# Kernel tuning notes

Measured on AMD Instinct MI355X. Metric: run time of the kernel, lower is better.

## Reference

```python
import jax, jax.numpy as jnp
import numpy as np

EMB = 1024
HEADS = 16
HD = EMB // HEADS

def setup_inputs() -> dict:
    key = jax.random.key(0)
    ks = jax.random.split(key, 9)
    s = 1.0 / np.sqrt(EMB)
    x = jax.random.normal(ks[0], (4, 2048, EMB), dtype=jnp.float32)
    Wq = jax.random.uniform(ks[1], (EMB, EMB), jnp.float32, -s, s)
    bq = jax.random.uniform(ks[2], (EMB,), jnp.float32, -s, s)
    Wk = jax.random.uniform(ks[3], (EMB, EMB), jnp.float32, -s, s)
    bk = jax.random.uniform(ks[4], (EMB,), jnp.float32, -s, s)
    Wv = jax.random.uniform(ks[5], (EMB, EMB), jnp.float32, -s, s)
    bv = jax.random.uniform(ks[6], (EMB,), jnp.float32, -s, s)
    Wo = jax.random.uniform(ks[7], (EMB, EMB), jnp.float32, -s, s)
    bo = jax.random.uniform(ks[8], (EMB,), jnp.float32, -s, s)
    return {"x": x, "Wq": Wq, "bq": bq, "Wk": Wk, "bk": bk, "Wv": Wv, "bv": bv, "Wo": Wo, "bo": bo}

def reference(x, Wq, bq, Wk, bk, Wv, bv, Wo, bo):
    B, T, C = x.shape
    # projections (torch Linear: y = x @ W^T + b)
    q = (x @ Wq.T + bq).reshape(B, T, HEADS, HD).transpose(0, 2, 1, 3)  # [B,H,T,hd]
    k = (x @ Wk.T + bk).reshape(B, T, HEADS, HD).transpose(0, 2, 1, 3)
    v = (x @ Wv.T + bv).reshape(B, T, HEADS, HD).transpose(0, 2, 1, 3)
    scores = jnp.einsum('bhqd,bhkd->bhqk', q, k) / jnp.sqrt(jnp.float32(HD))
    weights = jax.nn.softmax(scores, axis=-1)
    attn = jnp.einsum('bhqk,bhkd->bhqd', weights, v)
    out = attn.transpose(0, 2, 1, 3).reshape(B, T, C)
    return out @ Wo.T + bo
```

## Files before the change

kernel.cpp:

```cpp
#include <hip/hip_runtime.h>

#define TSEQ  2048
#define BATCH 4
#define NHEAD 16
#define EMB   1024

typedef __attribute__((ext_vector_type(8))) __bf16 bf16x8;
typedef __attribute__((ext_vector_type(4))) __bf16 bf16x4;
typedef __attribute__((ext_vector_type(4))) float  floatx4;
typedef __attribute__((ext_vector_type(2))) unsigned int uint32x2;
typedef __attribute__((ext_vector_type(4))) unsigned int uint32x4;

__device__ __forceinline__ void gload_lds16(const __bf16* g, __bf16* lds_uniform_base) {
  __builtin_amdgcn_global_load_lds(
      (__attribute__((address_space(1))) void*)(g),
      (__attribute__((address_space(3))) void*)(lds_uniform_base),
      16, 0, 0);
}

__global__ __launch_bounds__(256) void cvt_f32_bf16(
    const float* __restrict__ src, __bf16* __restrict__ dst)
{
  const int gid = (blockIdx.x * 256 + threadIdx.x) * 4;
  const float4 v = *(const float4*)(src + gid);
  dst[gid + 0] = (__bf16)v.x;
  dst[gid + 1] = (__bf16)v.y;
  dst[gid + 2] = (__bf16)v.z;
  dst[gid + 3] = (__bf16)v.w;
}

__global__ __launch_bounds__(256) void cvt_w4(
    const float* __restrict__ s0, const float* __restrict__ s1,
    const float* __restrict__ s2, const float* __restrict__ s3,
    __bf16* __restrict__ d0, __bf16* __restrict__ d1,
    __bf16* __restrict__ d2, __bf16* __restrict__ d3)
{
  const int z = blockIdx.z;
  const float* src = (z == 0) ? s0 : (z == 1) ? s1 : (z == 2) ? s2 : s3;
  __bf16*      dst = (z == 0) ? d0 : (z == 1) ? d1 : (z == 2) ? d2 : d3;
  const int gid = (blockIdx.x * 256 + threadIdx.x) * 4;
  const float4 v = *(const float4*)(src + gid);
  dst[gid + 0] = (__bf16)v.x;
  dst[gid + 1] = (__bf16)v.y;
  dst[gid + 2] = (__bf16)v.z;
  dst[gid + 3] = (__bf16)v.w;
}

#define GQ_NT 16

#define G2_STAGE(BUF, T)                                                                  \
  {                                                                                       \
    _Pragma("unroll")                                                                     \
    for (int c = 0; c < 4; c++)                                                           \
      gload_lds16(aStage + (size_t)(c * 64) * 1024 + (T) * 64,                            \
                  &As[BUF][(c * 64 + wid * 8) * 64]);                                     \
    _Pragma("unroll")                                                                     \
    for (int c = 0; c < 2; c++)                                                           \
      gload_lds16(bStage + (size_t)(c * 64) * 1024 + (T) * 64,                            \
                  &Bs[BUF][(c * 64 + wid * 8) * 64]);                                     \
  }

#define G2_AF(I, H) (*(const bf16x8*)(&As[cur][(wm * 64 + (I) * 16 + l16) * 64 + (((H) * 4 + quad) ^ h7) * 8]))
#define G2_BF(J, H) (*(const bf16x8*)(&Bs[cur][(wn * 64 + (J) * 16 + l16) * 64 + (((H) * 4 + quad) ^ h7) * 8]))

#define G2_MFMA_PAIR(I, J)                                                                \
  acc[I][J] = __builtin_amdgcn_mfma_f32_16x16x32_bf16(af[I][0], bfr[J][0], acc[I][J], 0, 0, 0); \
  acc[I][J] = __builtin_amdgcn_mfma_f32_16x16x32_bf16(af[I][1], bfr[J][1], acc[I][J], 0, 0, 0);

#define GEMM2_BODY(C_STORE)                                                               \
  const int tid  = threadIdx.x;                                                           \
  const int lane = tid & 63;                                                              \
  const int wid  = tid >> 6;                                                    \
  const int l16  = lane & 15;                                                             \
  const int quad = lane >> 4;                                                             \
  const int wm   = wid >> 1;                                        \
  const int wn   = wid & 1;                                         \
  const int lin  = blockIdx.x + blockIdx.y * 8;                                           \
  const int swz  = (lin & 7) * 32 + (lin >> 3);                                           \
  const int m0   = (swz >> 3) * 256;                                                      \
  const int n0   = (swz & 7) * 128;                                                       \
  __shared__ alignas(16) __bf16 As[2][256 * 64];                                          \
  __shared__ alignas(16) __bf16 Bs[2][128 * 64];                                          \
  floatx4 acc[4][4];                                                                      \
  _Pragma("unroll")                                                                       \
  for (int i = 0; i < 4; i++)                                                             \
    _Pragma("unroll")                                                                     \
    for (int j = 0; j < 4; j++) acc[i][j] = (floatx4){0.f, 0.f, 0.f, 0.f};                \
  const int lrow = lane >> 3;                                                             \
  const int xsg  = (lane & 7) ^ lrow;                                                     \
  const __bf16* aStage = A + (size_t)(m0 + wid * 8 + lrow) * 1024 + xsg * 8;              \
  const __bf16* bStage = W + (size_t)(n0 + wid * 8 + lrow) * 1024 + xsg * 8;              \
  const int h7 = l16 & 7;                                                                 \
  G2_STAGE(0, 0)                                                                          \
  G2_STAGE(1, 1)                                                                          \
  __asm__ __volatile__("s_waitcnt vmcnt(6)\n\ts_barrier" ::: "memory");                   \
  int cur = 0;                                                                            \
  _Pragma("unroll 1")                                                                     \
  for (int t = 0; t < GQ_NT; ++t) {                                                       \
    bf16x8 af[4][2], bfr[4][2];                                                           \
                                    \
    af[0][0] = G2_AF(0, 0);  af[0][1] = G2_AF(0, 1);                                      \
    af[1][0] = G2_AF(1, 0);  af[1][1] = G2_AF(1, 1);                                      \
    bfr[0][0] = G2_BF(0, 0); bfr[0][1] = G2_BF(0, 1);                                     \
    bfr[1][0] = G2_BF(1, 0); bfr[1][1] = G2_BF(1, 1);                                     \
    __builtin_amdgcn_s_setprio(1);                                                        \
    G2_MFMA_PAIR(0, 0) G2_MFMA_PAIR(0, 1) G2_MFMA_PAIR(1, 0) G2_MFMA_PAIR(1, 1)          \
    __builtin_amdgcn_s_setprio(0);                                                        \
    __asm__ __volatile__("s_barrier" ::: "memory");                                       \
                           \
    bfr[2][0] = G2_BF(2, 0); bfr[2][1] = G2_BF(2, 1);                                     \
    bfr[3][0] = G2_BF(3, 0); bfr[3][1] = G2_BF(3, 1);                                     \
    __builtin_amdgcn_s_setprio(1);                                                        \
    G2_MFMA_PAIR(0, 2) G2_MFMA_PAIR(0, 3) G2_MFMA_PAIR(1, 2) G2_MFMA_PAIR(1, 3)          \
    __builtin_amdgcn_s_setprio(0);                                                        \
    __asm__ __volatile__("s_barrier" ::: "memory");                                       \
                           \
    af[2][0] = G2_AF(2, 0);  af[2][1] = G2_AF(2, 1);                                      \
    af[3][0] = G2_AF(3, 0);  af[3][1] = G2_AF(3, 1);                                      \
    __builtin_amdgcn_s_setprio(1);                                                        \
    G2_MFMA_PAIR(2, 0) G2_MFMA_PAIR(2, 1) G2_MFMA_PAIR(3, 0) G2_MFMA_PAIR(3, 1)          \
    __builtin_amdgcn_s_setprio(0);                                                        \
    __asm__ __volatile__("s_barrier" ::: "memory");                                       \
                 \
                 \
    if (t + 2 < GQ_NT) { G2_STAGE(cur, t + 2) }                                           \
    __builtin_amdgcn_s_setprio(1);                                                        \
    G2_MFMA_PAIR(2, 2) G2_MFMA_PAIR(2, 3) G2_MFMA_PAIR(3, 2) G2_MFMA_PAIR(3, 3)          \
    __builtin_amdgcn_s_setprio(0);                                                        \
    if (t + 2 < GQ_NT) {                                                                  \
      __asm__ __volatile__("s_waitcnt vmcnt(6)\n\ts_barrier" ::: "memory");               \
    } else if (t + 1 < GQ_NT) {                                                           \
      __asm__ __volatile__("s_waitcnt vmcnt(0)\n\ts_barrier" ::: "memory");               \
    }                                                                                     \
    cur ^= 1;                                                                             \
  }                                                                                       \
  float bv[4];                                                                            \
  _Pragma("unroll")                                                                       \
  for (int j = 0; j < 4; j++) bv[j] = Bb[n0 + wn * 64 + j * 16 + l16];                    \
  _Pragma("unroll")                                                                       \
  for (int i = 0; i < 4; i++) {                                                           \
    const size_t mrow = (size_t)m0 + wm * 64 + i * 16 + quad * 4;                         \
    _Pragma("unroll")                                                                     \
    for (int j = 0; j < 4; j++) {                                                         \
      const int col = n0 + wn * 64 + j * 16 + l16;                                        \
      _Pragma("unroll")                                                                   \
      for (int r = 0; r < 4; r++) C_STORE;                                                \
    }                                                                                     \
  }

__global__ __launch_bounds__(512, 2) void gemm_bt_bias(
    const __bf16* __restrict__ A,
    const __bf16* __restrict__ W0, const __bf16* __restrict__ W1, const __bf16* __restrict__ W2,
    const float* __restrict__ B0, const float* __restrict__ B1, const float* __restrict__ B2,
    __bf16* __restrict__ C0, __bf16* __restrict__ C1, __bf16* __restrict__ C2)
{
  const int z = blockIdx.z;
  const __bf16* W  = (z == 0) ? W0 : ((z == 1) ? W1 : W2);
  const float*  Bb = (z == 0) ? B0 : ((z == 1) ? B1 : B2);
  __bf16*       C  = (z == 0) ? C0 : ((z == 1) ? C1 : C2);
  const float  scl = (z == 0) ? 0.125f * 1.44269504088896340736f : 1.0f;
  GEMM2_BODY(C[(mrow + r) * 1024 + col] = (__bf16)((acc[i][j][r] + bv[j]) * scl))
}

__global__ __launch_bounds__(512, 2) void gemm_bt_bias_f32(
    const __bf16* __restrict__ A, const __bf16* __restrict__ W,
    const float* __restrict__ Bb, float* __restrict__ C)
{
  GEMM2_BODY(C[(mrow + r) * 1024 + col] = acc[i][j][r] + bv[j])
}

__global__ __launch_bounds__(256) void v_transpose(
    const __bf16* __restrict__ V, __bf16* __restrict__ VT)
{
  const int t0 = blockIdx.x * 64;
  const int bh = blockIdx.y;
  const int b  = bh >> 4;
  const int h  = bh & 15;
  const int tid = threadIdx.x;

  __shared__ alignas(16) __bf16 Ls[64 * 72];

  const int row = tid >> 2, seg = tid & 3;
  const __bf16* src = V + ((size_t)(b * TSEQ + t0 + row)) * EMB + h * 64;
  *(bf16x8*)(&Ls[row * 72 + seg * 8])       = *(const bf16x8*)(src + seg * 8);
  *(bf16x8*)(&Ls[row * 72 + (seg + 4) * 8]) = *(const bf16x8*)(src + (seg + 4) * 8);
  __syncthreads();

  const int od = tid >> 2, oseg = tid & 3;
  bf16x8 o0, o1;
#pragma unroll
  for (int j = 0; j < 8; j++) o0[j] = Ls[(oseg * 16 + j) * 72 + od];
#pragma unroll
  for (int j = 0; j < 8; j++) o1[j] = Ls[(oseg * 16 + 8 + j) * 72 + od];
  __bf16* dst = VT + ((size_t)bh * 64 + od) * TSEQ + t0 + oseg * 16;
  *(bf16x8*)(dst)     = o0;
  *(bf16x8*)(dst + 8) = o1;
}

#define KVB 64
#define NT  (TSEQ / KVB)

#define FA_ZERO (floatx4){0.f, 0.f, 0.f, 0.f}

#define FA_STAGE(BUF, TILE)                                                               \
  if ((TILE) < NT) {                                                                      \
    _Pragma("unroll")                                                                     \
    for (int c = 0; c < 2; c++) {                                                         \
      gload_lds16(kstage + (size_t)((TILE) * KVB + c * 8) * EMB,                          \
                  &Ks[BUF][(wid * 16 + c * 8) * 64]);                                     \
      gload_lds16(vstage + (size_t)(c * 8) * TSEQ + (TILE) * KVB,                         \
                  &VTs[BUF][(wid * 16 + c * 8) * 64]);                                    \
    }                                                                                     \
  }

#define SM_PACK(TA, TB, DST)                                                              \
  {                                                                                       \
    bf16x4 pa_, pb_;                                                                      \
    _Pragma("unroll")                                                                     \
    for (int r = 0; r < 4; r++) pa_[r] = (__bf16)__builtin_amdgcn_exp2f((TA)[r]);         \
    _Pragma("unroll")                                                                     \
    for (int r = 0; r < 4; r++) pb_[r] = (__bf16)__builtin_amdgcn_exp2f((TB)[r]);         \
    const uint32x2 A2_ = __builtin_bit_cast(uint32x2, pa_);                               \
    const uint32x2 B2_ = __builtin_bit_cast(uint32x2, pb_);                               \
    const uint32x2 r0_ = __builtin_amdgcn_permlane32_swap(A2_.x, B2_.x, false, false);    \
    const uint32x2 r1_ = __builtin_amdgcn_permlane32_swap(A2_.y, B2_.y, false, false);    \
    const uint32x2 s0_ = __builtin_amdgcn_permlane16_swap(r0_.x, r0_.y, false, false);    \
    const uint32x2 s1_ = __builtin_amdgcn_permlane16_swap(r1_.x, r1_.y, false, false);    \
    const uint32x4 fw_ = (uint32x4){s0_.x, s1_.x, s0_.y, s1_.y};                          \
    DST = __builtin_bit_cast(bf16x8, fw_);                                                \
  }

#define QK_BLOCK(BUF, KS, TA, TB)                                                         \
  {                                                                                       \
    const bf16x8 ka0 = *(const bf16x8*)(&Ks[BUF][(KS) * 2048 + aoff0]);                   \
    const bf16x8 ka1 = *(const bf16x8*)(&Ks[BUF][(KS) * 2048 + aoff1]);                   \
    const bf16x8 kb0 = *(const bf16x8*)(&Ks[BUF][(KS) * 2048 + 1024 + aoff0]);            \
    const bf16x8 kb1 = *(const bf16x8*)(&Ks[BUF][(KS) * 2048 + 1024 + aoff1]);            \
    _Pragma("unroll")                                                                     \
    for (int g = 0; g < 4; g++) {                                                         \
      TA[g] = FA_ZERO;                                                                    \
      TA[g] = __builtin_amdgcn_mfma_f32_16x16x32_bf16(ka0, qf[g][0], TA[g], 0, 0, 0);     \
      TA[g] = __builtin_amdgcn_mfma_f32_16x16x32_bf16(ka1, qf[g][1], TA[g], 0, 0, 0);     \
      TB[g] = FA_ZERO;                                                                    \
      TB[g] = __builtin_amdgcn_mfma_f32_16x16x32_bf16(kb0, qf[g][0], TB[g], 0, 0, 0);     \
      TB[g] = __builtin_amdgcn_mfma_f32_16x16x32_bf16(kb1, qf[g][1], TB[g], 0, 0, 0);     \
    }                                                                                     \
  }

#define FA_STEP(BUF, KT)                                                                  \
  {                                                                                       \
    __builtin_amdgcn_s_setprio(1);                                                        \
    bf16x8 vf[4][2];                                                                      \
    _Pragma("unroll")                                                                     \
    for (int dg = 0; dg < 4; dg++) {                                                      \
      vf[dg][0] = *(const bf16x8*)(&VTs[(BUF) ^ 1][dg * 1024 + aoff0]);                   \
      vf[dg][1] = *(const bf16x8*)(&VTs[(BUF) ^ 1][dg * 1024 + aoff1]);                   \
    }                                                                                     \
    floatx4 ta[4], tb[4];                                                                 \
    QK_BLOCK(BUF, 0, ta, tb)                                                              \
    _Pragma("unroll")                                                                     \
    for (int g = 0; g < 4; g++) {                                                         \
      bf16x8 nf;                                                                          \
      SM_PACK(ta[g], tb[g], nf)                                                           \
      _Pragma("unroll")                                                                   \
      for (int dg = 0; dg < 4; dg++)                                                      \
        Oacc[g][dg] = __builtin_amdgcn_mfma_f32_16x16x32_bf16(vf[dg][0], pfragP[g][0], Oacc[g][dg], 0, 0, 0); \
      lacc[g] = __builtin_amdgcn_mfma_f32_16x16x32_bf16(ones, pfragP[g][0], lacc[g], 0, 0, 0); \
      _Pragma("unroll")                                                                   \
      for (int dg = 0; dg < 4; dg++)                                                      \
        Oacc[g][dg] = __builtin_amdgcn_mfma_f32_16x16x32_bf16(vf[dg][1], pfragP[g][1], Oacc[g][dg], 0, 0, 0); \
      lacc[g] = __builtin_amdgcn_mfma_f32_16x16x32_bf16(ones, pfragP[g][1], lacc[g], 0, 0, 0); \
      pfragP[g][0] = nf;                                                                  \
    }                                                                                     \
    QK_BLOCK(BUF, 1, ta, tb)                                                              \
    __builtin_amdgcn_s_setprio(0);                                                        \
    __syncthreads();                                                                      \
    FA_STAGE((BUF) ^ 1, (KT) + 1);                                                        \
    _Pragma("unroll")                                                                     \
    for (int g = 0; g < 4; g++) { SM_PACK(ta[g], tb[g], pfragP[g][1]) }                   \
    __syncthreads();                                                                      \
  }

__global__ __launch_bounds__(256, 2) void flash_attn(
    const __bf16* __restrict__ Q, const __bf16* __restrict__ K,
    const __bf16* __restrict__ VT, __bf16* __restrict__ O)
{
  const int lin = blockIdx.x + blockIdx.y * 8;
  const int swz = (lin & 7) * 64 + (lin >> 3);
  const int qt  = swz & 7;
  const int bh  = swz >> 3;
  const int b    = bh >> 4;
  const int h    = bh & 15;
  const int tid  = threadIdx.x;
  const int wid  = tid >> 6;
  const int lane = tid & 63;
  const int l16  = lane & 15;
  const int quad = lane >> 4;

  __shared__ alignas(16) __bf16 Ks[2][KVB * 64];
  __shared__ alignas(16) __bf16 VTs[2][64 * 64];

  const size_t base = ((size_t)b * TSEQ) * EMB + (size_t)h * 64;
  const __bf16* qptr  = Q + base;
  const __bf16* kptr  = K + base;
  const __bf16* vtptr = VT + (size_t)bh * 64 * TSEQ;
  __bf16*       optr  = O + base;

  const int qb = qt * 256 + wid * 64;

  bf16x8 qf[4][2];
#pragma unroll
  for (int g = 0; g < 4; g++)
#pragma unroll
    for (int hf = 0; hf < 2; hf++)
      qf[g][hf] = *(const bf16x8*)(qptr + (size_t)(qb + g * 16 + l16) * EMB + hf * 32 + quad * 8);

  floatx4 Oacc[4][4];
#pragma unroll
  for (int g = 0; g < 4; g++)
#pragma unroll
    for (int dg = 0; dg < 4; dg++) Oacc[g][dg] = FA_ZERO;
  floatx4 lacc[4];
#pragma unroll
  for (int g = 0; g < 4; g++) lacc[g] = FA_ZERO;

  const uint32x4 onesw = (uint32x4){0x3F803F80u, 0x3F803F80u, 0x3F803F80u, 0x3F803F80u};
  const bf16x8 ones = __builtin_bit_cast(bf16x8, onesw);

  const int lrow = lane >> 3;
  const int xsg  = (lane & 7) ^ lrow;
  const __bf16* kstage = kptr  + (size_t)(wid * 16 + lrow) * EMB  + xsg * 8;
  const __bf16* vstage = vtptr + (size_t)(wid * 16 + lrow) * TSEQ + xsg * 8;

  const int h7    = l16 & 7;
  const int x0    = quad ^ h7;
  const int aoff0 = l16 * 64 + x0 * 8;
  const int aoff1 = l16 * 64 + (x0 ^ 4) * 8;

  bf16x8 pfragP[4][2];

  FA_STAGE(0, 0);
  __syncthreads();
  FA_STAGE(1, 1);
  {
    floatx4 ta[4], tb[4];
    QK_BLOCK(0, 0, ta, tb)
#pragma unroll
    for (int g = 0; g < 4; g++) { SM_PACK(ta[g], tb[g], pfragP[g][0]) }
    QK_BLOCK(0, 1, ta, tb)
#pragma unroll
    for (int g = 0; g < 4; g++) { SM_PACK(ta[g], tb[g], pfragP[g][1]) }
  }
  __syncthreads();

#pragma unroll 1
  for (int kt = 1; kt < NT - 1; kt += 2) {
    FA_STEP(1, kt);
    FA_STEP(0, kt + 1);
  }
  FA_STEP(1, NT - 1);

#pragma unroll
  for (int g = 0; g < 4; g++) {
#pragma unroll
    for (int dg = 0; dg < 4; dg++) {
      const bf16x8 v0 = *(const bf16x8*)(&VTs[1][dg * 1024 + aoff0]);
      const bf16x8 v1 = *(const bf16x8*)(&VTs[1][dg * 1024 + aoff1]);
      Oacc[g][dg] = __builtin_amdgcn_mfma_f32_16x16x32_bf16(v0, pfragP[g][0], Oacc[g][dg], 0, 0, 0);
      Oacc[g][dg] = __builtin_amdgcn_mfma_f32_16x16x32_bf16(v1, pfragP[g][1], Oacc[g][dg], 0, 0, 0);
    }
    lacc[g] = __builtin_amdgcn_mfma_f32_16x16x32_bf16(ones, pfragP[g][0], lacc[g], 0, 0, 0);
    lacc[g] = __builtin_amdgcn_mfma_f32_16x16x32_bf16(ones, pfragP[g][1], lacc[g], 0, 0, 0);
  }

#pragma unroll
  for (int g = 0; g < 4; g++) {
    const float inv = 1.0f / lacc[g][0];
#pragma unroll
    for (int dg = 0; dg < 4; dg++) {
      bf16x4 ov;
#pragma unroll
      for (int r = 0; r < 4; r++) ov[r] = (__bf16)(Oacc[g][dg][r] * inv);
      *(bf16x4*)(optr + (size_t)(qb + g * 16 + l16) * EMB + dg * 16 + quad * 4) = ov;
    }
  }
}

extern "C" void kernel_launch(void* const* d_in, const int* in_sizes, int n_in,
                              void* d_out, int out_size, void* d_ws, size_t ws_size,
                              hipStream_t stream) {
  const float* x  = (const float*)d_in[0];
  const float* Wq = (const float*)d_in[1];
  const float* bq = (const float*)d_in[2];
  const float* Wk = (const float*)d_in[3];
  const float* bk = (const float*)d_in[4];
  const float* Wv = (const float*)d_in[5];
  const float* bv = (const float*)d_in[6];
  const float* Wo = (const float*)d_in[7];
  const float* bo = (const float*)d_in[8];
  float* out = (float*)d_out;

  const size_t NELEM = (size_t)BATCH * TSEQ * EMB;
  const size_t WELEM = (size_t)EMB * EMB;

  __bf16* q_b  = (__bf16*)d_out;
  __bf16* k_b  = q_b + NELEM;
  __bf16* x_b  = (__bf16*)d_ws;
  __bf16* v_b  = x_b + NELEM;
  __bf16* wq_b = v_b + NELEM;
  __bf16* wk_b = wq_b + WELEM;
  __bf16* wv_b = wk_b + WELEM;
  __bf16* wo_b = wv_b + WELEM;

  dim3 blk(256, 1, 1);
  dim3 blk512(512, 1, 1);

  cvt_f32_bf16<<<(int)(NELEM / 1024), blk, 0, stream>>>(x, x_b);
  cvt_w4<<<dim3((int)(WELEM / 1024), 1, 4), blk, 0, stream>>>(
      Wq, Wk, Wv, Wo, wq_b, wk_b, wv_b, wo_b);

  gemm_bt_bias<<<dim3(8, 32, 3), blk512, 0, stream>>>(
      x_b, wq_b, wk_b, wv_b, bq, bk, bv, q_b, k_b, v_b);

  v_transpose<<<dim3(TSEQ / 64, BATCH * NHEAD), blk, 0, stream>>>(v_b, x_b);

  flash_attn<<<dim3(TSEQ / 256, BATCH * NHEAD), blk, 0, stream>>>(
      q_b, k_b, x_b, v_b);

  gemm_bt_bias_f32<<<dim3(8, 32, 1), blk512, 0, stream>>>(v_b, wo_b, bo, out);
}
```

Baseline: 271.7 us.

## Replace 256x128 GEMM with simpler 128x128 tile double-buffered kernel

Rewrites the projection GEMMs to use 128x128 output tiles per 256-thread block with a 32-wide K step and a simple one-ahead double buffer. This replaces the 512-thread 256x128 tile, the 64-wide K step and the two-stage-ahead prefetch with interleaved barriers. The grids are doubled in the M dimension to match. Smaller blocks may improve scheduling flexibility, but they lower data reuse per tile and double the number of barrier-synchronised K iterations.

New measurement: 262.7 us. -3.3%, faster.

```diff
diff --git a/kernel.cpp b/kernel.cpp
--- a/kernel.cpp
+++ b/kernel.cpp
@@ -46,90 +46,66 @@
   dst[gid + 3] = (__bf16)v.w;
 }
 
-#define GQ_NT 16
-
-#define G2_STAGE(BUF, T)                                                                  \
+#define GK_NT 32
+
+#define G_STAGE(BUF, K0)                                                                  \
   {                                                                                       \
     _Pragma("unroll")                                                                     \
-    for (int c = 0; c < 4; c++)                                                           \
-      gload_lds16(aStage + (size_t)(c * 64) * 1024 + (T) * 64,                            \
-                  &As[BUF][(c * 64 + wid * 8) * 64]);                                     \
-    _Pragma("unroll")                                                                     \
-    for (int c = 0; c < 2; c++)                                                           \
-      gload_lds16(bStage + (size_t)(c * 64) * 1024 + (T) * 64,                            \
-                  &Bs[BUF][(c * 64 + wid * 8) * 64]);                                     \
-  }
-
-#define G2_AF(I, H) (*(const bf16x8*)(&As[cur][(wm * 64 + (I) * 16 + l16) * 64 + (((H) * 4 + quad) ^ h7) * 8]))
-#define G2_BF(J, H) (*(const bf16x8*)(&Bs[cur][(wn * 64 + (J) * 16 + l16) * 64 + (((H) * 4 + quad) ^ h7) * 8]))
-
-#define G2_MFMA_PAIR(I, J)                                                                \
-  acc[I][J] = __builtin_amdgcn_mfma_f32_16x16x32_bf16(af[I][0], bfr[J][0], acc[I][J], 0, 0, 0); \
-  acc[I][J] = __builtin_amdgcn_mfma_f32_16x16x32_bf16(af[I][1], bfr[J][1], acc[I][J], 0, 0, 0);
-
-#define GEMM2_BODY(C_STORE)                                                               \
+    for (int is = 0; is < 2; is++) {                                                      \
+      gload_lds16(aStage + (size_t)(is * 64) * 1024 + (K0),                               \
+                  &As[BUF][(is * 256 + wid * 64) * 8]);                                   \
+      gload_lds16(bStage + (size_t)(is * 64) * 1024 + (K0),                               \
+                  &Bs[BUF][(is * 256 + wid * 64) * 8]);                                   \
+    }                                                                                     \
+  }
+
+#define GEMM_BODY(C_STORE)                                                                \
   const int tid  = threadIdx.x;                                                           \
   const int lane = tid & 63;                                                              \
-  const int wid  = tid >> 6;                                                    \
+  const int wid  = tid >> 6;                                                              \
   const int l16  = lane & 15;                                                             \
   const int quad = lane >> 4;                                                             \
-  const int wm   = wid >> 1;                                        \
-  const int wn   = wid & 1;                                         \
+  const int wm   = wid & 1;                                                               \
+  const int wn   = wid >> 1;                                                              \
   const int lin  = blockIdx.x + blockIdx.y * 8;                                           \
-  const int swz  = (lin & 7) * 32 + (lin >> 3);                                           \
-  const int m0   = (swz >> 3) * 256;                                                      \
+  const int swz  = (lin & 7) * 64 + (lin >> 3);                                           \
+  const int m0   = (swz >> 3) * 128;                                                      \
   const int n0   = (swz & 7) * 128;                                                       \
-  __shared__ alignas(16) __bf16 As[2][256 * 64];                                          \
-  __shared__ alignas(16) __bf16 Bs[2][128 * 64];                                          \
+  __shared__ alignas(16) __bf16 As[2][128 * 32];                                          \
+  __shared__ alignas(16) __bf16 Bs[2][128 * 32];                                          \
   floatx4 acc[4][4];                                                                      \
   _Pragma("unroll")                                                                       \
   for (int i = 0; i < 4; i++)                                                             \
     _Pragma("unroll")                                                                     \
     for (int j = 0; j < 4; j++) acc[i][j] = (floatx4){0.f, 0.f, 0.f, 0.f};                \
-  const int lrow = lane >> 3;                                                             \
-  const int xsg  = (lane & 7) ^ lrow;                                                     \
-  const __bf16* aStage = A + (size_t)(m0 + wid * 8 + lrow) * 1024 + xsg * 8;              \
-  const __bf16* bStage = W + (size_t)(n0 + wid * 8 + lrow) * 1024 + xsg * 8;              \
-  const int h7 = l16 & 7;                                                                 \
-  G2_STAGE(0, 0)                                                                          \
-  G2_STAGE(1, 1)                                                                          \
-  __asm__ __volatile__("s_waitcnt vmcnt(6)\n\ts_barrier" ::: "memory");                   \
+                      \
+                     \
+  const int srow = tid >> 2;                                                              \
+  const int xsg  = (tid & 3) ^ (srow & 3);                                                \
+  const __bf16* aStage = A + (size_t)(m0 + srow) * 1024 + xsg * 8;                        \
+  const __bf16* bStage = W + (size_t)(n0 + srow) * 1024 + xsg * 8;                        \
+                      \
+  const int xq = quad ^ (l16 & 3);                                                        \
+  G_STAGE(0, 0)                                                                           \
+  __asm__ __volatile__("s_waitcnt vmcnt(0)\n\ts_barrier" ::: "memory");                   \
   int cur = 0;                                                                            \
   _Pragma("unroll 1")                                                                     \
-  for (int t = 0; t < GQ_NT; ++t) {                                                       \
-    bf16x8 af[4][2], bfr[4][2];                                                           \
-                                    \
-    af[0][0] = G2_AF(0, 0);  af[0][1] = G2_AF(0, 1);                                      \
-    af[1][0] = G2_AF(1, 0);  af[1][1] = G2_AF(1, 1);                                      \
-    bfr[0][0] = G2_BF(0, 0); bfr[0][1] = G2_BF(0, 1);                                     \
-    bfr[1][0] = G2_BF(1, 0); bfr[1][1] = G2_BF(1, 1);                                     \
+  for (int k = 0; k < GK_NT; ++k) {                                                       \
+    if (k + 1 < GK_NT) { G_STAGE(cur ^ 1, (k + 1) * 32) }                                 \
+    bf16x8 af[4], bfr[4];                                                                 \
+    _Pragma("unroll")                                                                     \
+    for (int i = 0; i < 4; i++) {                                                         \
+      af[i]  = *(const bf16x8*)(&As[cur][(wm * 64 + i * 16 + l16) * 32 + xq * 8]);        \
+      bfr[i] = *(const bf16x8*)(&Bs[cur][(wn * 64 + i * 16 + l16) * 32 + xq * 8]);        \
+    }                                                                                     \
     __builtin_amdgcn_s_setprio(1);                                                        \
-    G2_MFMA_PAIR(0, 0) G2_MFMA_PAIR(0, 1) G2_MFMA_PAIR(1, 0) G2_MFMA_PAIR(1, 1)          \
+    _Pragma("unroll")                                                                     \
+    for (int i = 0; i < 4; i++)                                                           \
+      _Pragma("unroll")                                                                   \
+      for (int j = 0; j < 4; j++)                                                         \
+        acc[i][j] = __builtin_amdgcn_mfma_f32_16x16x32_bf16(af[i], bfr[j], acc[i][j], 0, 0, 0); \
     __builtin_amdgcn_s_setprio(0);                                                        \
-    __asm__ __volatile__("s_barrier" ::: "memory");                                       \
-                           \
-    bfr[2][0] = G2_BF(2, 0); bfr[2][1] = G2_BF(2, 1);                                     \
-    bfr[3][0] = G2_BF(3, 0); bfr[3][1] = G2_BF(3, 1);                                     \
-    __builtin_amdgcn_s_setprio(1);                                                        \
-    G2_MFMA_PAIR(0, 2) G2_MFMA_PAIR(0, 3) G2_MFMA_PAIR(1, 2) G2_MFMA_PAIR(1, 3)          \
-    __builtin_amdgcn_s_setprio(0);                                                        \
-    __asm__ __volatile__("s_barrier" ::: "memory");                                       \
-                           \
-    af[2][0] = G2_AF(2, 0);  af[2][1] = G2_AF(2, 1);                                      \
-    af[3][0] = G2_AF(3, 0);  af[3][1] = G2_AF(3, 1);                                      \
-    __builtin_amdgcn_s_setprio(1);                                                        \
-    G2_MFMA_PAIR(2, 0) G2_MFMA_PAIR(2, 1) G2_MFMA_PAIR(3, 0) G2_MFMA_PAIR(3, 1)          \
-    __builtin_amdgcn_s_setprio(0);                                                        \
-    __asm__ __volatile__("s_barrier" ::: "memory");                                       \
-                 \
-                 \
-    if (t + 2 < GQ_NT) { G2_STAGE(cur, t + 2) }                                           \
-    __builtin_amdgcn_s_setprio(1);                                                        \
-    G2_MFMA_PAIR(2, 2) G2_MFMA_PAIR(2, 3) G2_MFMA_PAIR(3, 2) G2_MFMA_PAIR(3, 3)          \
-    __builtin_amdgcn_s_setprio(0);                                                        \
-    if (t + 2 < GQ_NT) {                                                                  \
-      __asm__ __volatile__("s_waitcnt vmcnt(6)\n\ts_barrier" ::: "memory");               \
-    } else if (t + 1 < GQ_NT) {                                                           \
+    if (k + 1 < GK_NT) {                                                                  \
       __asm__ __volatile__("s_waitcnt vmcnt(0)\n\ts_barrier" ::: "memory");               \
     }                                                                                     \
     cur ^= 1;                                                                             \
@@ -148,7 +124,7 @@
     }                                                                                     \
   }
 
-__global__ __launch_bounds__(512, 2) void gemm_bt_bias(
+__global__ __launch_bounds__(256) void gemm_bt_bias(
     const __bf16* __restrict__ A,
     const __bf16* __restrict__ W0, const __bf16* __restrict__ W1, const __bf16* __restrict__ W2,
     const float* __restrict__ B0, const float* __restrict__ B1, const float* __restrict__ B2,
@@ -159,14 +135,14 @@
   const float*  Bb = (z == 0) ? B0 : ((z == 1) ? B1 : B2);
   __bf16*       C  = (z == 0) ? C0 : ((z == 1) ? C1 : C2);
   const float  scl = (z == 0) ? 0.125f * 1.44269504088896340736f : 1.0f;
-  GEMM2_BODY(C[(mrow + r) * 1024 + col] = (__bf16)((acc[i][j][r] + bv[j]) * scl))
-}
-
-__global__ __launch_bounds__(512, 2) void gemm_bt_bias_f32(
+  GEMM_BODY(C[(mrow + r) * 1024 + col] = (__bf16)((acc[i][j][r] + bv[j]) * scl))
+}
+
+__global__ __launch_bounds__(256) void gemm_bt_bias_f32(
     const __bf16* __restrict__ A, const __bf16* __restrict__ W,
     const float* __restrict__ Bb, float* __restrict__ C)
 {
-  GEMM2_BODY(C[(mrow + r) * 1024 + col] = acc[i][j][r] + bv[j])
+  GEMM_BODY(C[(mrow + r) * 1024 + col] = acc[i][j][r] + bv[j])
 }
 
 __global__ __launch_bounds__(256) void v_transpose(
@@ -413,13 +389,12 @@
   __bf16* wo_b = wv_b + WELEM;
 
   dim3 blk(256, 1, 1);
-  dim3 blk512(512, 1, 1);
 
   cvt_f32_bf16<<<(int)(NELEM / 1024), blk, 0, stream>>>(x, x_b);
   cvt_w4<<<dim3((int)(WELEM / 1024), 1, 4), blk, 0, stream>>>(
       Wq, Wk, Wv, Wo, wq_b, wk_b, wv_b, wo_b);
 
-  gemm_bt_bias<<<dim3(8, 32, 3), blk512, 0, stream>>>(
+  gemm_bt_bias<<<dim3(8, 64, 3), blk, 0, stream>>>(
       x_b, wq_b, wk_b, wv_b, bq, bk, bv, q_b, k_b, v_b);
 
   v_transpose<<<dim3(TSEQ / 64, BATCH * NHEAD), blk, 0, stream>>>(v_b, x_b);
@@ -427,5 +402,5 @@
   flash_attn<<<dim3(TSEQ / 256, BATCH * NHEAD), blk, 0, stream>>>(
       q_b, k_b, x_b, v_b);
 
-  gemm_bt_bias_f32<<<dim3(8, 32, 1), blk512, 0, stream>>>(v_b, wo_b, bo, out);
-}
+  gemm_bt_bias_f32<<<dim3(8, 64, 1), blk, 0, stream>>>(v_b, wo_b, bo, out);
+}
```
